# Optimization experiments

Measured on AMD Instinct MI355X. Metric: run time of the kernel, lower is better.

## Reference

```python
import jax, jax.numpy as jnp
import numpy as np

B, N, IN_F, OUT_F, OP_D = 64, 96, 128, 128, 48
SKIP_IDX = 1
ATTN_SCALE = 1.0


def setup_inputs() -> dict:
    key = jax.random.key(0)
    ks = jax.random.split(key, 7)
    return {
        "inputs": jax.random.normal(ks[0], (B, N, IN_F), dtype=jnp.float32),
        "adj": jax.random.randint(ks[1], (B, N, N), 0, 5, dtype=jnp.int64),
        "op_emb": jax.random.normal(ks[2], (B, N, N, OP_D), dtype=jnp.float32),
        "weight": jax.random.normal(ks[3], (IN_F, OUT_F), dtype=jnp.float32) * (1.0 / np.sqrt(OUT_F)),
        "attn_w": jax.random.normal(ks[4], (OP_D, OUT_F), dtype=jnp.float32) * (1.0 / np.sqrt(OP_D)),
        "attn_b": jax.random.normal(ks[5], (OUT_F,), dtype=jnp.float32) * 0.01,
        "self_op_emb": jax.random.normal(ks[6], (OP_D,), dtype=jnp.float32),
    }


def reference(inputs, adj, op_emb, weight, attn_w, attn_b, self_op_emb):
    # support: [B, N, OUT_F]
    support = jnp.matmul(inputs, weight)
    n = adj.shape[-1]
    eye = jnp.eye(n, dtype=bool)  # [N, N]
    # plus_I: replace diagonal op embeddings with self_op_emb, add I to adj
    op_emb = jnp.where(eye[..., None], self_op_emb, op_emb)  # [B,N,N,OP_D]
    adj = adj + eye.astype(adj.dtype)
    # attention over op embeddings: [B,N,N,OUT_F]
    attn = jax.nn.sigmoid(jnp.matmul(op_emb, attn_w) + attn_b)
    attn = (adj != 0)[..., None].astype(attn.dtype) * attn * ATTN_SCALE
    # skip-connection edges get attention == 1
    is_skip = (adj == SKIP_IDX)[..., None].astype(attn.dtype)
    attn = is_skip + (1.0 - is_skip) * attn
    # processed_info = sum_j attn[b,i,j,:] * support[b,j,:]; residual = support
    processed_info = jnp.einsum("bijd,bjd->bid", attn, support)
    return processed_info + support
```

## Files before the change

### kernel.cpp

```cpp
#include <hip/hip_runtime.h>
#include <hip/hip_bf16.h>


#define B_ 64
#define N_ 96
#define F_ 128
#define D_ 48
#define G_ 12
#define NGRP (N_ / G_)

typedef __attribute__((ext_vector_type(8))) short short8;
typedef __attribute__((ext_vector_type(4))) float f32x4;

#if __has_builtin(__builtin_amdgcn_exp2f)
#define EXP2(x) __builtin_amdgcn_exp2f(x)
#else
#define EXP2(x) exp2f(x)
#endif

__device__ __forceinline__ void gload_lds16(const void* g, void* l) {
    __builtin_amdgcn_global_load_lds(
        (const __attribute__((address_space(1))) void*)g,
        (__attribute__((address_space(3))) void*)l, 16, 0, 0);
}

__device__ __forceinline__ size_t s2i(int b, int mt, int r, int lg, int fbp) {
    return ((((size_t)b * 6 + mt) * 4 + r) * 4 + lg) * 64 + fbp;
}

__device__ __forceinline__ unsigned bfbits(float x) {
    union { __hip_bfloat16 h; unsigned short u; } cv;
    cv.h = __float2bfloat16(x);
    return (unsigned)cv.u;
}

__global__ __launch_bounds__(256, 4) void support_kernel(
    const float* __restrict__ inputs, const float* __restrict__ weight,
    float2* __restrict__ S2)
{
    __shared__ float in_lds[16 * F_];
    const int tid = threadIdx.x;
    const int row0 = blockIdx.x * 16;
    ((float4*)in_lds)[tid]       = ((const float4*)(inputs + (size_t)row0 * F_))[tid];
    ((float4*)in_lds)[tid + 256] = ((const float4*)(inputs + (size_t)row0 * F_))[tid + 256];
    __syncthreads();
    const int rl = tid >> 4, f0 = (tid & 15) * 8;
    float acc[8] = {0.f,0.f,0.f,0.f,0.f,0.f,0.f,0.f};
    #pragma unroll 4
    for (int k = 0; k < F_; ++k) {
        const float a = in_lds[rl * F_ + k];
        const float4 w0 = *(const float4*)(weight + k * F_ + f0);
        const float4 w1 = *(const float4*)(weight + k * F_ + f0 + 4);
        acc[0] += a * w0.x; acc[1] += a * w0.y; acc[2] += a * w0.z; acc[3] += a * w0.w;
        acc[4] += a * w1.x; acc[5] += a * w1.y; acc[6] += a * w1.z; acc[7] += a * w1.w;
    }
    const int R = row0 + rl;
    const int b = R / N_, j = R - b * N_;
    const int mt = j >> 4, lg = (j >> 2) & 3, r = j & 3;
    #pragma unroll
    for (int q = 0; q < 4; ++q) {
        const int fbp = (f0 >> 1) + q;
        S2[s2i(b, mt, r, lg, fbp)] = make_float2(acc[2 * q], acc[2 * q + 1]);
    }
}

__global__ __launch_bounds__(512, 4) void fused_kernel(
    const float* __restrict__ op_emb,
    const unsigned* __restrict__ adjw,
    const float* __restrict__ attn_w,
    const float* __restrict__ attn_b,
    const float* __restrict__ self_op,
    const float2* __restrict__ S2,
    float* __restrict__ out)
{
    __shared__ __align__(16) float F32buf[3][N_ * D_];
    __shared__ __align__(16) unsigned short Atile[N_ * 64];
    __shared__ __align__(8)  float2 Ppart[2][4][16];
    __shared__ unsigned short moff[G_][N_];

    const int tid  = threadIdx.x;
    const int lane = tid & 63;
    const int wid  = tid >> 6;
    const int wf   = wid & 3;
    const int wj   = wid >> 2;
    const int lg   = lane >> 4;
    const int lm   = lane & 15;
    const int fb   = wf * 32 + lm * 2;
    const int fbp  = wf * 16 + lm;

    const int blk = blockIdx.x;
    const int b   = blk / NGRP;
    const int grp = blk - b * NGRP;
    const int i0  = grp * G_;

    const float kNL2E = -1.44269504088896f;

    const unsigned probe = adjw[2 * lane + 1];
    const bool use32 = __any(probe != 0);

    auto issue_tile = [&](int i, int pb) {
        const char* gbase = (const char*)(op_emb + (size_t)(b * N_ + i) * N_ * D_);
        char* lbase = (char*)(&F32buf[pb][0]);
        #pragma unroll
        for (int c0 = 0; c0 < 3; ++c0) {
            int c = wid + 8 * c0;
            c = (c < 18) ? c : 17;
            gload_lds16(gbase + c * 1024 + lane * 16, lbase + c * 1024);
        }
    };

    issue_tile(i0, 0);
    issue_tile(i0 + 1, 1);

    #pragma unroll 1
    for (int g = 0; g < G_; ++g) {
        if (tid < N_) {
            const int i = i0 + g;
            const size_t idx = (size_t)(b * N_ + i) * N_ + tid;
            int a = use32 ? (int)adjw[idx] : (int)adjw[2 * idx];
            a += (tid == i) ? 1 : 0;
            const float off = (a == 0) ? 126.f : ((a == 1) ? -126.f : 0.f);
            moff[g][tid] = (unsigned short)bfbits(off);
        }
    }

    short8 bfrag[2][2];
    float  bbias[2];
    {
        const float2 bb = *(const float2*)(attn_b + fb);
        bbias[0] = bb.x * kNL2E;
        bbias[1] = bb.y * kNL2E;
        #pragma unroll
        for (int ks = 0; ks < 2; ++ks) {
            short8 v0, v1;
            #pragma unroll
            for (int e = 0; e < 8; ++e) {
                const int d = ks * 32 + lg * 8 + e;
                if (d < D_) {
                    const float2 w = *(const float2*)(attn_w + d * F_ + fb);
                    v0[e] = (short)bfbits(w.x * kNL2E);
                    v1[e] = (short)bfbits(w.y * kNL2E);
                } else {
                    const unsigned one = (d == D_) ? bfbits(1.0f) : 0u;
                    v0[e] = (short)one;
                    v1[e] = (short)one;
                }
            }
            bfrag[0][ks] = v0;
            bfrag[1][ks] = v1;
        }
    }

    float2 sfrag[3][4];
    #pragma unroll
    for (int s = 0; s < 3; ++s)
        #pragma unroll
        for (int r = 0; r < 4; ++r)
            sfrag[s][r] = S2[s2i(b, 3 * wj + s, r, lg, fbp)];

    for (int v = tid; v < N_ * 7; v += 512) {
        const int j = v / 7, q = v - 7 * j;
        const int byte = j * 128 + ((100 + q * 4) ^ ((j & 7) << 4));
        *(unsigned*)((char*)Atile + byte) = 0u;
    }

    __syncthreads();

    float osum_prev0 = 0.f, osum_prev1 = 0.f;

    #pragma unroll 1
    for (int g = 0; g < G_; ++g) {
        const int i = i0 + g;

        {
            const int inext = i0 + ((g + 2 < G_) ? (g + 2) : (G_ - 1));
            issue_tile(inext, (g + 2) % 3);
        }

        asm volatile("s_waitcnt vmcnt(6) lgkmcnt(0)" ::: "memory");
        __builtin_amdgcn_s_barrier();

        if (g > 0 && wj == 0 && lg == 0) {
            const int ip = i - 1;
            const float2 pp = Ppart[(g - 1) & 1][wf][lm];
            const float2 sr = S2[s2i(b, ip >> 4, ip & 3, (ip >> 2) & 3, fbp)];
            float2 o;
            o.x = osum_prev0 + pp.x + sr.x;
            o.y = osum_prev1 + pp.y + sr.y;
            *(float2*)(out + (size_t)(b * N_ + ip) * F_ + fb) = o;
        }

        {
            const float* fsrc = &F32buf[g % 3][0];
            #pragma unroll
            for (int s = 0; s < 3; ++s) {
                const int w = tid + s * 512;
                if (w < N_ * 12) {
                    const int j = w / 12, c = w - 12 * j;
                    float4 p;
                    if (j == i) p = *(const float4*)(self_op + c * 4);
                    else        p = *(const float4*)((const char*)fsrc + 16 * w);
                    const int byte = j * 128 + ((c * 8) ^ ((j & 7) << 4));
                    *(uint2*)((char*)Atile + byte) =
                        make_uint2(bfbits(p.x) | (bfbits(p.y) << 16),
                                   bfbits(p.z) | (bfbits(p.w) << 16));
                }
            }
            if (tid < N_) {
                const int byte = tid * 128 + (96 ^ ((tid & 7) << 4));
                *(unsigned*)((char*)Atile + byte) = (unsigned)moff[g][tid];
            }
        }
        asm volatile("s_waitcnt lgkmcnt(0)" ::: "memory");
        __builtin_amdgcn_s_barrier();

        float osum0 = 0.f, osum1 = 0.f;
        #pragma unroll
        for (int s = 0; s < 3; ++s) {
            const int mt  = 3 * wj + s;
            const int jr  = mt * 16 + lm;
            const int swz = (lm & 7) << 4;
            const char* base = (const char*)Atile + jr * 128;
            const short8 a0 = *(const short8*)(base + (( 0 + lg * 16) ^ swz));
            const short8 a1 = *(const short8*)(base + ((64 + lg * 16) ^ swz));
            f32x4 c0 = (f32x4){bbias[0], bbias[0], bbias[0], bbias[0]};
            f32x4 c1 = (f32x4){bbias[1], bbias[1], bbias[1], bbias[1]};
            c0 = __builtin_amdgcn_mfma_f32_16x16x32_bf16(a0, bfrag[0][0], c0, 0, 0, 0);
            c0 = __builtin_amdgcn_mfma_f32_16x16x32_bf16(a1, bfrag[0][1], c0, 0, 0, 0);
            c1 = __builtin_amdgcn_mfma_f32_16x16x32_bf16(a0, bfrag[1][0], c1, 0, 0, 0);
            c1 = __builtin_amdgcn_mfma_f32_16x16x32_bf16(a1, bfrag[1][1], c1, 0, 0, 0);
            #pragma unroll
            for (int r = 0; r < 4; ++r) {
                const float s0 = __builtin_amdgcn_rcpf(1.f + EXP2(c0[r]));
                const float s1 = __builtin_amdgcn_rcpf(1.f + EXP2(c1[r]));
                osum0 = __builtin_fmaf(s0, sfrag[s][r].x, osum0);
                osum1 = __builtin_fmaf(s1, sfrag[s][r].y, osum1);
            }
        }
        osum0 += __shfl_xor(osum0, 16);
        osum0 += __shfl_xor(osum0, 32);
        osum1 += __shfl_xor(osum1, 16);
        osum1 += __shfl_xor(osum1, 32);
        if (wj == 1 && lg == 0)
            Ppart[g & 1][wf][lm] = make_float2(osum0, osum1);
        osum_prev0 = osum0;
        osum_prev1 = osum1;
    }

    asm volatile("s_waitcnt lgkmcnt(0)" ::: "memory");
    __builtin_amdgcn_s_barrier();
    if (wj == 0 && lg == 0) {
        const int ip = i0 + G_ - 1;
        const float2 pp = Ppart[(G_ - 1) & 1][wf][lm];
        const float2 sr = S2[s2i(b, ip >> 4, ip & 3, (ip >> 2) & 3, fbp)];
        float2 o;
        o.x = osum_prev0 + pp.x + sr.x;
        o.y = osum_prev1 + pp.y + sr.y;
        *(float2*)(out + (size_t)(b * N_ + ip) * F_ + fb) = o;
    }
}

extern "C" void kernel_launch(void* const* d_in, const int* in_sizes, int n_in,
                              void* d_out, int out_size, void* d_ws, size_t ws_size,
                              hipStream_t stream) {
    const float*    inputs  = (const float*)d_in[0];
    const unsigned* adjw    = (const unsigned*)d_in[1];
    const float*    op_emb  = (const float*)d_in[2];
    const float*    weight  = (const float*)d_in[3];
    const float*    attn_w  = (const float*)d_in[4];
    const float*    attn_b  = (const float*)d_in[5];
    const float*    self_op = (const float*)d_in[6];
    float* out = (float*)d_out;
    float2* S2 = (float2*)d_ws;

    support_kernel<<<(B_ * N_) / 16, 256, 0, stream>>>(inputs, weight, S2);
    fused_kernel<<<B_ * NGRP, 512, 0, stream>>>(op_emb, adjw, attn_w, attn_b, self_op,
                                                S2, out);
}
```

Before: 61.92 us.

## Process attention rows in pairs with double-buffered A tiles

Switches the op_emb staging from a triple to a double buffer and double-buffers the bf16 A tile. The MFMA and sigmoid reduction now runs once per pair of rows, covering both tiles, which halves the number of compute phases and merges the output writes. The adjacency mask precompute is spread across all threads instead of a serial per-row loop. The trade-offs are a shallower prefetch depth (one tile ahead instead of two) and higher register pressure from the paired accumulators.

New measurement: 72.40 us. 16.9% more time.

```diff
diff --git a/kernel.cpp b/kernel.cpp
--- a/kernel.cpp
+++ b/kernel.cpp
@@ -73,9 +73,9 @@
     const float2* __restrict__ S2,
     float* __restrict__ out)
 {
-    __shared__ __align__(16) float F32buf[3][N_ * D_];
-    __shared__ __align__(16) unsigned short Atile[N_ * 64];
-    __shared__ __align__(8)  float2 Ppart[2][4][16];
+    __shared__ __align__(16) float F32buf[2][N_ * D_];
+    __shared__ __align__(16) unsigned short Atile[2][N_ * 64];
+    __shared__ __align__(8)  float2 Ppart[2][2][4][16];
     __shared__ unsigned short moff[G_][N_];
 
     const int tid  = threadIdx.x;
@@ -110,18 +110,15 @@
     };
 
     issue_tile(i0, 0);
-    issue_tile(i0 + 1, 1);
-
-    #pragma unroll 1
-    for (int g = 0; g < G_; ++g) {
-        if (tid < N_) {
-            const int i = i0 + g;
-            const size_t idx = (size_t)(b * N_ + i) * N_ + tid;
-            int a = use32 ? (int)adjw[idx] : (int)adjw[2 * idx];
-            a += (tid == i) ? 1 : 0;
-            const float off = (a == 0) ? 126.f : ((a == 1) ? -126.f : 0.f);
-            moff[g][tid] = (unsigned short)bfbits(off);
-        }
+
+    for (int v = tid; v < G_ * N_; v += 512) {
+        const int g = v / N_, j = v - g * N_;
+        const int i = i0 + g;
+        const size_t idx = (size_t)(b * N_ + i) * N_ + j;
+        int a = use32 ? (int)adjw[idx] : (int)adjw[2 * idx];
+        a += (j == i) ? 1 : 0;
+        const float off = (a == 0) ? 126.f : ((a == 1) ? -126.f : 0.f);
+        moff[g][j] = (unsigned short)bfbits(off);
     }
 
     short8 bfrag[2][2];
@@ -158,40 +155,46 @@
         for (int r = 0; r < 4; ++r)
             sfrag[s][r] = S2[s2i(b, 3 * wj + s, r, lg, fbp)];
 
-    for (int v = tid; v < N_ * 7; v += 512) {
-        const int j = v / 7, q = v - 7 * j;
+    for (int v = tid; v < 2 * N_ * 7; v += 512) {
+        const int t = v / (N_ * 7);
+        const int vv = v - t * (N_ * 7);
+        const int j = vv / 7, q = vv - 7 * j;
         const int byte = j * 128 + ((100 + q * 4) ^ ((j & 7) << 4));
-        *(unsigned*)((char*)Atile + byte) = 0u;
+        *(unsigned*)((char*)(&Atile[t][0]) + byte) = 0u;
     }
 
     __syncthreads();
 
-    float osum_prev0 = 0.f, osum_prev1 = 0.f;
+    float osumP[2][2] = {{0.f, 0.f}, {0.f, 0.f}};
 
     #pragma unroll 1
     for (int g = 0; g < G_; ++g) {
+        const int cur = g & 1;
         const int i = i0 + g;
 
+        if ((g & 1) && g >= 3 && wj == 0 && lg == 0) {
+            #pragma unroll
+            for (int tt = 0; tt < 2; ++tt) {
+                const int ip = i - 3 + tt;
+                const float2 pp = Ppart[((g - 2) >> 1) & 1][tt][wf][lm];
+                const float2 sr = S2[s2i(b, ip >> 4, ip & 3, (ip >> 2) & 3, fbp)];
+                float2 o;
+                o.x = osumP[tt][0] + pp.x + sr.x;
+                o.y = osumP[tt][1] + pp.y + sr.y;
+                *(float2*)(out + (size_t)(b * N_ + ip) * F_ + fb) = o;
+            }
+        }
+
         {
-            const int inext = i0 + ((g + 2 < G_) ? (g + 2) : (G_ - 1));
-            issue_tile(inext, (g + 2) % 3);
-        }
-
-        asm volatile("s_waitcnt vmcnt(6) lgkmcnt(0)" ::: "memory");
+            const int inx = (g + 1 < G_) ? (g + 1) : (G_ - 1);
+            issue_tile(i0 + inx, (g + 1) & 1);
+        }
+
+        asm volatile("s_waitcnt vmcnt(3)" ::: "memory");
         __builtin_amdgcn_s_barrier();
 
-        if (g > 0 && wj == 0 && lg == 0) {
-            const int ip = i - 1;
-            const float2 pp = Ppart[(g - 1) & 1][wf][lm];
-            const float2 sr = S2[s2i(b, ip >> 4, ip & 3, (ip >> 2) & 3, fbp)];
-            float2 o;
-            o.x = osum_prev0 + pp.x + sr.x;
-            o.y = osum_prev1 + pp.y + sr.y;
-            *(float2*)(out + (size_t)(b * N_ + ip) * F_ + fb) = o;
-        }
-
         {
-            const float* fsrc = &F32buf[g % 3][0];
+            const float* fsrc = &F32buf[cur][0];
             #pragma unroll
             for (int s = 0; s < 3; ++s) {
                 const int w = tid + s * 512;
@@ -201,62 +204,74 @@
                     if (j == i) p = *(const float4*)(self_op + c * 4);
                     else        p = *(const float4*)((const char*)fsrc + 16 * w);
                     const int byte = j * 128 + ((c * 8) ^ ((j & 7) << 4));
-                    *(uint2*)((char*)Atile + byte) =
+                    *(uint2*)((char*)(&Atile[cur][0]) + byte) =
                         make_uint2(bfbits(p.x) | (bfbits(p.y) << 16),
                                    bfbits(p.z) | (bfbits(p.w) << 16));
                 }
             }
             if (tid < N_) {
                 const int byte = tid * 128 + (96 ^ ((tid & 7) << 4));
-                *(unsigned*)((char*)Atile + byte) = (unsigned)moff[g][tid];
+                *(unsigned*)((char*)(&Atile[cur][0]) + byte) = (unsigned)moff[g][tid];
             }
         }
         asm volatile("s_waitcnt lgkmcnt(0)" ::: "memory");
         __builtin_amdgcn_s_barrier();
 
-        float osum0 = 0.f, osum1 = 0.f;
-        #pragma unroll
-        for (int s = 0; s < 3; ++s) {
-            const int mt  = 3 * wj + s;
-            const int jr  = mt * 16 + lm;
-            const int swz = (lm & 7) << 4;
-            const char* base = (const char*)Atile + jr * 128;
-            const short8 a0 = *(const short8*)(base + (( 0 + lg * 16) ^ swz));
-            const short8 a1 = *(const short8*)(base + ((64 + lg * 16) ^ swz));
-            f32x4 c0 = (f32x4){bbias[0], bbias[0], bbias[0], bbias[0]};
-            f32x4 c1 = (f32x4){bbias[1], bbias[1], bbias[1], bbias[1]};
-            c0 = __builtin_amdgcn_mfma_f32_16x16x32_bf16(a0, bfrag[0][0], c0, 0, 0, 0);
-            c0 = __builtin_amdgcn_mfma_f32_16x16x32_bf16(a1, bfrag[0][1], c0, 0, 0, 0);
-            c1 = __builtin_amdgcn_mfma_f32_16x16x32_bf16(a0, bfrag[1][0], c1, 0, 0, 0);
-            c1 = __builtin_amdgcn_mfma_f32_16x16x32_bf16(a1, bfrag[1][1], c1, 0, 0, 0);
-            #pragma unroll
-            for (int r = 0; r < 4; ++r) {
-                const float s0 = __builtin_amdgcn_rcpf(1.f + EXP2(c0[r]));
-                const float s1 = __builtin_amdgcn_rcpf(1.f + EXP2(c1[r]));
-                osum0 = __builtin_fmaf(s0, sfrag[s][r].x, osum0);
-                osum1 = __builtin_fmaf(s1, sfrag[s][r].y, osum1);
-            }
-        }
-        osum0 += __shfl_xor(osum0, 16);
-        osum0 += __shfl_xor(osum0, 32);
-        osum1 += __shfl_xor(osum1, 16);
-        osum1 += __shfl_xor(osum1, 32);
-        if (wj == 1 && lg == 0)
-            Ppart[g & 1][wf][lm] = make_float2(osum0, osum1);
-        osum_prev0 = osum0;
-        osum_prev1 = osum1;
+        if (g & 1) {
+            float osum[2][2] = {{0.f, 0.f}, {0.f, 0.f}};
+            #pragma unroll
+            for (int s = 0; s < 3; ++s) {
+                const int mt  = 3 * wj + s;
+                const int jr  = mt * 16 + lm;
+                const int swz = (lm & 7) << 4;
+                #pragma unroll
+                for (int tt = 0; tt < 2; ++tt) {
+                    const char* base = (const char*)(&Atile[tt][0]) + jr * 128;
+                    const short8 a0 = *(const short8*)(base + (( 0 + lg * 16) ^ swz));
+                    const short8 a1 = *(const short8*)(base + ((64 + lg * 16) ^ swz));
+                    f32x4 c0 = (f32x4){bbias[0], bbias[0], bbias[0], bbias[0]};
+                    f32x4 c1 = (f32x4){bbias[1], bbias[1], bbias[1], bbias[1]};
+                    c0 = __builtin_amdgcn_mfma_f32_16x16x32_bf16(a0, bfrag[0][0], c0, 0, 0, 0);
+                    c0 = __builtin_amdgcn_mfma_f32_16x16x32_bf16(a1, bfrag[0][1], c0, 0, 0, 0);
+                    c1 = __builtin_amdgcn_mfma_f32_16x16x32_bf16(a0, bfrag[1][0], c1, 0, 0, 0);
+                    c1 = __builtin_amdgcn_mfma_f32_16x16x32_bf16(a1, bfrag[1][1], c1, 0, 0, 0);
+                    #pragma unroll
+                    for (int r = 0; r < 4; ++r) {
+                        const float s0 = __builtin_amdgcn_rcpf(1.f + EXP2(c0[r]));
+                        const float s1 = __builtin_amdgcn_rcpf(1.f + EXP2(c1[r]));
+                        osum[tt][0] = __builtin_fmaf(s0, sfrag[s][r].x, osum[tt][0]);
+                        osum[tt][1] = __builtin_fmaf(s1, sfrag[s][r].y, osum[tt][1]);
+                    }
+                }
+            }
+            #pragma unroll
+            for (int tt = 0; tt < 2; ++tt) {
+                float v0 = osum[tt][0], v1 = osum[tt][1];
+                v0 += __shfl_xor(v0, 16);
+                v0 += __shfl_xor(v0, 32);
+                v1 += __shfl_xor(v1, 16);
+                v1 += __shfl_xor(v1, 32);
+                if (wj == 1 && lg == 0)
+                    Ppart[(g >> 1) & 1][tt][wf][lm] = make_float2(v0, v1);
+                osumP[tt][0] = v0;
+                osumP[tt][1] = v1;
+            }
+        }
     }
 
     asm volatile("s_waitcnt lgkmcnt(0)" ::: "memory");
     __builtin_amdgcn_s_barrier();
     if (wj == 0 && lg == 0) {
-        const int ip = i0 + G_ - 1;
-        const float2 pp = Ppart[(G_ - 1) & 1][wf][lm];
-        const float2 sr = S2[s2i(b, ip >> 4, ip & 3, (ip >> 2) & 3, fbp)];
-        float2 o;
-        o.x = osum_prev0 + pp.x + sr.x;
-        o.y = osum_prev1 + pp.y + sr.y;
-        *(float2*)(out + (size_t)(b * N_ + ip) * F_ + fb) = o;
+        #pragma unroll
+        for (int tt = 0; tt < 2; ++tt) {
+            const int ip = i0 + G_ - 2 + tt;
+            const float2 pp = Ppart[((G_ - 1) >> 1) & 1][tt][wf][lm];
+            const float2 sr = S2[s2i(b, ip >> 4, ip & 3, (ip >> 2) & 3, fbp)];
+            float2 o;
+            o.x = osumP[tt][0] + pp.x + sr.x;
+            o.y = osumP[tt][1] + pp.y + sr.y;
+            *(float2*)(out + (size_t)(b * N_ + ip) * F_ + fb) = o;
+        }
     }
 }
 
```

## Build MFMA A-fragments straight from rotated f32 LDS tiles, dropping Atile stage

Applied to the files above, without the earlier changes.

The bf16 Atile staging buffer and its second barrier per row are removed. The global→LDS loads now write op_emb rows with a per-row chunk rotation so that MFMA lanes can read f32 fragments directly from LDS and pack them to bf16 in registers. The adjacency mask offset moves from a bias column inside the MFMA to a per-output add before exp2. Prefetch depth drops from two tiles ahead to one, trading some latency hiding for one fewer LDS pass and one fewer barrier per iteration.

Measured after the change: 91.37 us. 1.48x slower.

```diff
diff --git a/kernel.cpp b/kernel.cpp
--- a/kernel.cpp
+++ b/kernel.cpp
@@ -32,6 +32,15 @@
     union { __hip_bfloat16 h; unsigned short u; } cv;
     cv.h = __float2bfloat16(x);
     return (unsigned)cv.u;
+}
+
+__device__ __forceinline__ short8 pack8(float4 lo, float4 hi) {
+    short8 v;
+    v[0] = (short)bfbits(lo.x); v[1] = (short)bfbits(lo.y);
+    v[2] = (short)bfbits(lo.z); v[3] = (short)bfbits(lo.w);
+    v[4] = (short)bfbits(hi.x); v[5] = (short)bfbits(hi.y);
+    v[6] = (short)bfbits(hi.z); v[7] = (short)bfbits(hi.w);
+    return v;
 }
 
 __global__ __launch_bounds__(256, 4) void support_kernel(
@@ -74,9 +83,8 @@
     float* __restrict__ out)
 {
     __shared__ __align__(16) float F32buf[3][N_ * D_];
-    __shared__ __align__(16) unsigned short Atile[N_ * 64];
+    __shared__ __align__(16) float moff_f[G_][N_];
     __shared__ __align__(8)  float2 Ppart[2][4][16];
-    __shared__ unsigned short moff[G_][N_];
 
     const int tid  = threadIdx.x;
     const int lane = tid & 63;
@@ -98,30 +106,35 @@
     const unsigned probe = adjw[2 * lane + 1];
     const bool use32 = __any(probe != 0);
 
+    int goff[3], cchunk[3];
+    #pragma unroll
+    for (int c0 = 0; c0 < 3; ++c0) {
+        int c = wid + 8 * c0;
+        c = (c < 18) ? c : 17;
+        cchunk[c0] = c;
+        const int o16 = c * 64 + lane;
+        const int j = o16 / 12, v = o16 - 12 * j;
+        int u = v - (j % 12);
+        u = (u < 0) ? u + 12 : u;
+        goff[c0] = j * 192 + u * 16;
+    }
     auto issue_tile = [&](int i, int pb) {
         const char* gbase = (const char*)(op_emb + (size_t)(b * N_ + i) * N_ * D_);
         char* lbase = (char*)(&F32buf[pb][0]);
         #pragma unroll
-        for (int c0 = 0; c0 < 3; ++c0) {
-            int c = wid + 8 * c0;
-            c = (c < 18) ? c : 17;
-            gload_lds16(gbase + c * 1024 + lane * 16, lbase + c * 1024);
-        }
+        for (int c0 = 0; c0 < 3; ++c0)
+            gload_lds16(gbase + goff[c0], lbase + cchunk[c0] * 1024);
     };
 
     issue_tile(i0, 0);
-    issue_tile(i0 + 1, 1);
-
-    #pragma unroll 1
-    for (int g = 0; g < G_; ++g) {
-        if (tid < N_) {
-            const int i = i0 + g;
-            const size_t idx = (size_t)(b * N_ + i) * N_ + tid;
-            int a = use32 ? (int)adjw[idx] : (int)adjw[2 * idx];
-            a += (tid == i) ? 1 : 0;
-            const float off = (a == 0) ? 126.f : ((a == 1) ? -126.f : 0.f);
-            moff[g][tid] = (unsigned short)bfbits(off);
-        }
+
+    for (int v = tid; v < G_ * N_; v += 512) {
+        const int g = v / N_, j = v - g * N_;
+        const int i = i0 + g;
+        const size_t idx = (size_t)(b * N_ + i) * N_ + j;
+        int a = use32 ? (int)adjw[idx] : (int)adjw[2 * idx];
+        a += (j == i) ? 1 : 0;
+        moff_f[g][j] = (a == 0) ? 126.f : ((a == 1) ? -126.f : 0.f);
     }
 
     short8 bfrag[2][2];
@@ -141,9 +154,7 @@
                     v0[e] = (short)bfbits(w.x * kNL2E);
                     v1[e] = (short)bfbits(w.y * kNL2E);
                 } else {
-                    const unsigned one = (d == D_) ? bfbits(1.0f) : 0u;
-                    v0[e] = (short)one;
-                    v1[e] = (short)one;
+                    v0[e] = 0; v1[e] = 0;
                 }
             }
             bfrag[0][ks] = v0;
@@ -158,10 +169,20 @@
         for (int r = 0; r < 4; ++r)
             sfrag[s][r] = S2[s2i(b, 3 * wj + s, r, lg, fbp)];
 
-    for (int v = tid; v < N_ * 7; v += 512) {
-        const int j = v / 7, q = v - 7 * j;
-        const int byte = j * 128 + ((100 + q * 4) ^ ((j & 7) << 4));
-        *(unsigned*)((char*)Atile + byte) = 0u;
+    int aoff[3][4];
+    #pragma unroll
+    for (int s = 0; s < 3; ++s) {
+        const int mt = 3 * wj + s;
+        const int jrow = mt * 16 + lm;
+        const int jm = jrow % 12;
+        #pragma unroll
+        for (int q = 0; q < 4; ++q) {
+            const int u0 = (q < 2) ? (lg * 2 + q) : (8 + (lg & 1) * 2 + (q - 2));
+            int v = u0 + jm;
+            v = (v >= 12) ? v - 12 : v;
+            v = (v >= 12) ? v - 12 : v;
+            aoff[s][q] = jrow * 192 + v * 16;
+        }
     }
 
     __syncthreads();
@@ -173,11 +194,11 @@
         const int i = i0 + g;
 
         {
-            const int inext = i0 + ((g + 2 < G_) ? (g + 2) : (G_ - 1));
-            issue_tile(inext, (g + 2) % 3);
-        }
-
-        asm volatile("s_waitcnt vmcnt(6) lgkmcnt(0)" ::: "memory");
+            const int inx = (g + 1 < G_) ? (g + 1) : (G_ - 1);
+            issue_tile(i0 + inx, (g + 1) % 3);
+        }
+
+        asm volatile("s_waitcnt vmcnt(3) lgkmcnt(0)" ::: "memory");
         __builtin_amdgcn_s_barrier();
 
         if (g > 0 && wj == 0 && lg == 0) {
@@ -190,49 +211,45 @@
             *(float2*)(out + (size_t)(b * N_ + ip) * F_ + fb) = o;
         }
 
-        {
-            const float* fsrc = &F32buf[g % 3][0];
-            #pragma unroll
-            for (int s = 0; s < 3; ++s) {
-                const int w = tid + s * 512;
-                if (w < N_ * 12) {
-                    const int j = w / 12, c = w - 12 * j;
-                    float4 p;
-                    if (j == i) p = *(const float4*)(self_op + c * 4);
-                    else        p = *(const float4*)((const char*)fsrc + 16 * w);
-                    const int byte = j * 128 + ((c * 8) ^ ((j & 7) << 4));
-                    *(uint2*)((char*)Atile + byte) =
-                        make_uint2(bfbits(p.x) | (bfbits(p.y) << 16),
-                                   bfbits(p.z) | (bfbits(p.w) << 16));
+        const char* fb_ = (const char*)(&F32buf[g % 3][0]);
+        float osum0 = 0.f, osum1 = 0.f;
+        #pragma unroll
+        for (int s = 0; s < 3; ++s) {
+            const int mt = 3 * wj + s;
+            const int jrow = mt * 16 + lm;
+            const bool diag = (jrow == i);
+            float4 lo0, hi0;
+            if (diag) {
+                lo0 = *(const float4*)(self_op + lg * 8);
+                hi0 = *(const float4*)(self_op + lg * 8 + 4);
+            } else {
+                lo0 = *(const float4*)(fb_ + aoff[s][0]);
+                hi0 = *(const float4*)(fb_ + aoff[s][1]);
+            }
+            const short8 a0 = pack8(lo0, hi0);
+            short8 a1 = (short8){0,0,0,0,0,0,0,0};
+            if (lg < 2) {
+                float4 lo1, hi1;
+                if (diag) {
+                    lo1 = *(const float4*)(self_op + 32 + lg * 8);
+                    hi1 = *(const float4*)(self_op + 32 + lg * 8 + 4);
+                } else {
+                    lo1 = *(const float4*)(fb_ + aoff[s][2]);
+                    hi1 = *(const float4*)(fb_ + aoff[s][3]);
                 }
-            }
-            if (tid < N_) {
-                const int byte = tid * 128 + (96 ^ ((tid & 7) << 4));
-                *(unsigned*)((char*)Atile + byte) = (unsigned)moff[g][tid];
-            }
-        }
-        asm volatile("s_waitcnt lgkmcnt(0)" ::: "memory");
-        __builtin_amdgcn_s_barrier();
-
-        float osum0 = 0.f, osum1 = 0.f;
-        #pragma unroll
-        for (int s = 0; s < 3; ++s) {
-            const int mt  = 3 * wj + s;
-            const int jr  = mt * 16 + lm;
-            const int swz = (lm & 7) << 4;
-            const char* base = (const char*)Atile + jr * 128;
-            const short8 a0 = *(const short8*)(base + (( 0 + lg * 16) ^ swz));
-            const short8 a1 = *(const short8*)(base + ((64 + lg * 16) ^ swz));
+                a1 = pack8(lo1, hi1);
+            }
             f32x4 c0 = (f32x4){bbias[0], bbias[0], bbias[0], bbias[0]};
             f32x4 c1 = (f32x4){bbias[1], bbias[1], bbias[1], bbias[1]};
             c0 = __builtin_amdgcn_mfma_f32_16x16x32_bf16(a0, bfrag[0][0], c0, 0, 0, 0);
             c0 = __builtin_amdgcn_mfma_f32_16x16x32_bf16(a1, bfrag[0][1], c0, 0, 0, 0);
             c1 = __builtin_amdgcn_mfma_f32_16x16x32_bf16(a0, bfrag[1][0], c1, 0, 0, 0);
             c1 = __builtin_amdgcn_mfma_f32_16x16x32_bf16(a1, bfrag[1][1], c1, 0, 0, 0);
+            const f32x4 offv = *(const f32x4*)(&moff_f[g][mt * 16 + lg * 4]);
             #pragma unroll
             for (int r = 0; r < 4; ++r) {
-                const float s0 = __builtin_amdgcn_rcpf(1.f + EXP2(c0[r]));
-                const float s1 = __builtin_amdgcn_rcpf(1.f + EXP2(c1[r]));
+                const float s0 = __builtin_amdgcn_rcpf(1.f + EXP2(c0[r] + offv[r]));
+                const float s1 = __builtin_amdgcn_rcpf(1.f + EXP2(c1[r] + offv[r]));
                 osum0 = __builtin_fmaf(s0, sfrag[s][r].x, osum0);
                 osum1 = __builtin_fmaf(s1, sfrag[s][r].y, osum1);
             }
```

## Double-buffer bf16 A tile and convert next tile during current MFMA step

Applied to the files above, without the earlier changes.

Doubles the bf16 Atile in LDS so each iteration converts tile g+1 from the fp32 staging buffer while the MFMA and sigmoid work runs on tile g. This cuts the loop from two barriers per iteration to one. The adjacency mask is now packed into a 2-bit-per-row register code instead of a per-group LDS table. Each wave uses its own vmcnt count and there is no barrier between the wait and the read of other waves' async LDS loads, so the staging-buffer reads may race.

Measured after the change: 59.75 us. 1.04x faster.

```diff
diff --git a/kernel.cpp b/kernel.cpp
--- a/kernel.cpp
+++ b/kernel.cpp
@@ -74,9 +74,8 @@
     float* __restrict__ out)
 {
     __shared__ __align__(16) float F32buf[3][N_ * D_];
-    __shared__ __align__(16) unsigned short Atile[N_ * 64];
+    __shared__ __align__(16) unsigned short Atile[2][N_ * 64];
     __shared__ __align__(8)  float2 Ppart[2][4][16];
-    __shared__ unsigned short moff[G_][N_];
 
     const int tid  = threadIdx.x;
     const int lane = tid & 63;
@@ -112,15 +111,15 @@
     issue_tile(i0, 0);
     issue_tile(i0 + 1, 1);
 
-    #pragma unroll 1
-    for (int g = 0; g < G_; ++g) {
-        if (tid < N_) {
-            const int i = i0 + g;
-            const size_t idx = (size_t)(b * N_ + i) * N_ + tid;
+    unsigned mcode = 0;
+    if (tid < N_) {
+        #pragma unroll
+        for (int g2 = 0; g2 < G_; ++g2) {
+            const size_t idx = (size_t)(b * N_ + i0 + g2) * N_ + tid;
             int a = use32 ? (int)adjw[idx] : (int)adjw[2 * idx];
-            a += (tid == i) ? 1 : 0;
-            const float off = (a == 0) ? 126.f : ((a == 1) ? -126.f : 0.f);
-            moff[g][tid] = (unsigned short)bfbits(off);
+            a += (tid == i0 + g2) ? 1 : 0;
+            const unsigned code = (a == 0) ? 0u : ((a == 1) ? 1u : 2u);
+            mcode |= code << (2 * g2);
         }
     }
 
@@ -158,13 +157,44 @@
         for (int r = 0; r < 4; ++r)
             sfrag[s][r] = S2[s2i(b, 3 * wj + s, r, lg, fbp)];
 
-    for (int v = tid; v < N_ * 7; v += 512) {
-        const int j = v / 7, q = v - 7 * j;
+    for (int v = tid; v < 2 * N_ * 7; v += 512) {
+        const int t = v / (N_ * 7);
+        const int vv = v - t * (N_ * 7);
+        const int j = vv / 7, q = vv - 7 * j;
         const int byte = j * 128 + ((100 + q * 4) ^ ((j & 7) << 4));
-        *(unsigned*)((char*)Atile + byte) = 0u;
+        *(unsigned*)((char*)(&Atile[t][0]) + byte) = 0u;
     }
 
     __syncthreads();
+
+    auto convert_tile = [&](int gg) {
+        const int ic = i0 + gg;
+        const float* fsrc = &F32buf[gg % 3][0];
+        #pragma unroll
+        for (int s = 0; s < 3; ++s) {
+            const int w = tid + s * 512;
+            if (w < N_ * 12) {
+                const int j = w / 12, c = w - 12 * j;
+                float4 p;
+                if (j == ic) p = *(const float4*)(self_op + c * 4);
+                else         p = *(const float4*)((const char*)fsrc + 16 * w);
+                const int byte = j * 128 + ((c * 8) ^ ((j & 7) << 4));
+                *(uint2*)((char*)(&Atile[gg & 1][0]) + byte) =
+                    make_uint2(bfbits(p.x) | (bfbits(p.y) << 16),
+                               bfbits(p.z) | (bfbits(p.w) << 16));
+            }
+        }
+        if (tid < N_) {
+            const unsigned code = (mcode >> (2 * gg)) & 3u;
+            const unsigned bits = (code == 0) ? 0x42FCu : ((code == 1) ? 0xC2FCu : 0u);
+            const int byte = tid * 128 + (96 ^ ((tid & 7) << 4));
+            *(unsigned*)((char*)(&Atile[gg & 1][0]) + byte) = bits;
+        }
+    };
+
+    convert_tile(0);
+    asm volatile("s_waitcnt lgkmcnt(0)" ::: "memory");
+    __builtin_amdgcn_s_barrier();
 
     float osum_prev0 = 0.f, osum_prev1 = 0.f;
 
@@ -172,47 +202,27 @@
     for (int g = 0; g < G_; ++g) {
         const int i = i0 + g;
 
+        if (wj == 0 && lg == 0) {
+            const int ip = (g > 0) ? (i - 1) : i0;
+            const float2 srv = S2[s2i(b, ip >> 4, ip & 3, (ip >> 2) & 3, fbp)];
+            if (g > 0) {
+                const float2 pp = Ppart[(g - 1) & 1][wf][lm];
+                float2 o;
+                o.x = osum_prev0 + pp.x + srv.x;
+                o.y = osum_prev1 + pp.y + srv.y;
+                *(float2*)(out + (size_t)(b * N_ + ip) * F_ + fb) = o;
+            }
+        }
+
         {
-            const int inext = i0 + ((g + 2 < G_) ? (g + 2) : (G_ - 1));
-            issue_tile(inext, (g + 2) % 3);
-        }
-
-        asm volatile("s_waitcnt vmcnt(6) lgkmcnt(0)" ::: "memory");
-        __builtin_amdgcn_s_barrier();
-
-        if (g > 0 && wj == 0 && lg == 0) {
-            const int ip = i - 1;
-            const float2 pp = Ppart[(g - 1) & 1][wf][lm];
-            const float2 sr = S2[s2i(b, ip >> 4, ip & 3, (ip >> 2) & 3, fbp)];
-            float2 o;
-            o.x = osum_prev0 + pp.x + sr.x;
-            o.y = osum_prev1 + pp.y + sr.y;
-            *(float2*)(out + (size_t)(b * N_ + ip) * F_ + fb) = o;
-        }
-
-        {
-            const float* fsrc = &F32buf[g % 3][0];
-            #pragma unroll
-            for (int s = 0; s < 3; ++s) {
-                const int w = tid + s * 512;
-                if (w < N_ * 12) {
-                    const int j = w / 12, c = w - 12 * j;
-                    float4 p;
-                    if (j == i) p = *(const float4*)(self_op + c * 4);
-                    else        p = *(const float4*)((const char*)fsrc + 16 * w);
-                    const int byte = j * 128 + ((c * 8) ^ ((j & 7) << 4));
-                    *(uint2*)((char*)Atile + byte) =
-                        make_uint2(bfbits(p.x) | (bfbits(p.y) << 16),
-                                   bfbits(p.z) | (bfbits(p.w) << 16));
-                }
-            }
-            if (tid < N_) {
-                const int byte = tid * 128 + (96 ^ ((tid & 7) << 4));
-                *(unsigned*)((char*)Atile + byte) = (unsigned)moff[g][tid];
-            }
-        }
-        asm volatile("s_waitcnt lgkmcnt(0)" ::: "memory");
-        __builtin_amdgcn_s_barrier();
+            const int inx = (g + 2 < G_) ? (g + 2) : (G_ - 1);
+            issue_tile(i0 + inx, (g + 2) % 3);
+        }
+
+        if (wj == 0) asm volatile("s_waitcnt vmcnt(4)" ::: "memory");
+        else         asm volatile("s_waitcnt vmcnt(3)" ::: "memory");
+
+        convert_tile(g + 1);
 
         float osum0 = 0.f, osum1 = 0.f;
         #pragma unroll
@@ -220,7 +230,7 @@
             const int mt  = 3 * wj + s;
             const int jr  = mt * 16 + lm;
             const int swz = (lm & 7) << 4;
-            const char* base = (const char*)Atile + jr * 128;
+            const char* base = (const char*)(&Atile[g & 1][0]) + jr * 128;
             const short8 a0 = *(const short8*)(base + (( 0 + lg * 16) ^ swz));
             const short8 a1 = *(const short8*)(base + ((64 + lg * 16) ^ swz));
             f32x4 c0 = (f32x4){bbias[0], bbias[0], bbias[0], bbias[0]};
@@ -245,10 +255,11 @@
             Ppart[g & 1][wf][lm] = make_float2(osum0, osum1);
         osum_prev0 = osum0;
         osum_prev1 = osum1;
-    }
-
-    asm volatile("s_waitcnt lgkmcnt(0)" ::: "memory");
-    __builtin_amdgcn_s_barrier();
+
+        asm volatile("s_waitcnt lgkmcnt(0)" ::: "memory");
+        __builtin_amdgcn_s_barrier();
+    }
+
     if (wj == 0 && lg == 0) {
         const int ip = i0 + G_ - 1;
         const float2 pp = Ppart[(G_ - 1) & 1][wf][lm];
```
